# Kernel optimization log

Hardware: AMD Instinct MI355X
Metric: run time of the kernel (lower is better)

## Reference

```python
import jax, jax.numpy as jnp
import numpy as np

DIM = 1024
NUM_HEADS = 16
HEAD_DIM = DIM // NUM_HEADS


def _rope_tables(seq_len, dim, dtype):
    # matches llama_rotary_embedding: inv_freq over even indices of head_dim
    inv_freq = 1.0 / (10000.0 ** (jnp.arange(0, dim, 2, dtype=jnp.float32) / dim))
    t = jnp.arange(seq_len, dtype=jnp.float32)
    freqs = jnp.outer(t, inv_freq)  # [S, dim/2]
    return jnp.cos(freqs).astype(dtype), jnp.sin(freqs).astype(dtype)


def _apply_rope(x, cos_emb, sin_emb):
    # x: [B, H, S, hd]; takes interleaved halves, concatenates rotated halves
    x1 = x[..., 0::2]
    x2 = x[..., 1::2]
    return jnp.concatenate((x1 * cos_emb - x2 * sin_emb,
                            x1 * sin_emb + x2 * cos_emb), axis=-1)


def setup_inputs() -> dict:
    key = jax.random.key(0)
    k_x, k_qkv, k_out, k_b = jax.random.split(key, 4)
    B, S, D = 2, 2048, DIM
    x = jax.random.normal(k_x, (B, S, D), dtype=jnp.float32)
    # torch nn.Linear weights are [out_features, in_features]
    w_qkv = jax.random.normal(k_qkv, (3 * D, D), dtype=jnp.float32) * (1.0 / np.sqrt(D))
    w_out = jax.random.normal(k_out, (D, D), dtype=jnp.float32) * (1.0 / np.sqrt(D))
    b_out = jax.random.normal(k_b, (D,), dtype=jnp.float32) * 0.01
    return {"x": x, "w_qkv": w_qkv, "w_out": w_out, "b_out": b_out}


def reference(x, w_qkv, w_out, b_out):
    B, S, D = x.shape
    H, hd = NUM_HEADS, HEAD_DIM
    qkv = jnp.einsum('bsd,ed->bse', x, w_qkv)  # [B, S, 3D]
    q, k, v = jnp.split(qkv, 3, axis=-1)
    # [B, S, D] -> [B, H, S, hd]
    q, k, v = (t.reshape(B, S, H, hd).transpose(0, 2, 1, 3) for t in (q, k, v))
    cos_emb, sin_emb = _rope_tables(S, hd, x.dtype)  # [S, hd/2]
    q = _apply_rope(q, cos_emb, sin_emb)
    k = _apply_rope(k, cos_emb, sin_emb)
    scores = jnp.einsum('bhqd,bhkd->bhqk', q, k) / jnp.sqrt(jnp.asarray(hd, x.dtype))
    attn = jax.nn.softmax(scores, axis=-1)
    out = jnp.einsum('bhqk,bhkd->bhqd', attn, v)
    out = out.transpose(0, 2, 1, 3).reshape(B, S, D)
    return jnp.einsum('bsd,ed->bse', out, w_out) + b_out
```

## Files before the change

kernel.cpp:

```cpp
#include <hip/hip_runtime.h>
#include <math.h>

typedef __bf16 bf16_t;
typedef bf16_t bf16x8 __attribute__((ext_vector_type(8)));
typedef bf16_t bf16x4 __attribute__((ext_vector_type(4)));
typedef short  s16x4  __attribute__((ext_vector_type(4)));
typedef float  f32x4  __attribute__((ext_vector_type(4)));

#define DIM_   1024
#define NHEADS 16
#define HDIM   64
#define SEQ    2048
#define BATCH  2

#define QK_SCALE 0.18033688011112042f
#define ROPE_LF 0.41524101186092029f

__device__ __forceinline__ s16x4 as_s16x4(bf16x4 v) {
    union { bf16x4 b; s16x4 s; } u; u.b = v; return u.s;
}

__device__ __forceinline__ void gld16(const bf16_t* g, bf16_t* l) {
    __builtin_amdgcn_global_load_lds(
        (const __attribute__((address_space(1))) void*)g,
        (__attribute__((address_space(3))) void*)l, 16, 0, 0);
}

#define XCNT   (4096u * 1024u)
#define WQCNT  (3072u * 1024u)
#define WOCNT  (1024u * 1024u)
__global__ __launch_bounds__(256) void cast3(const float* __restrict__ s0,
                                             const float* __restrict__ s1,
                                             const float* __restrict__ s2,
                                             bf16_t* __restrict__ d0,
                                             bf16_t* __restrict__ d1,
                                             bf16_t* __restrict__ d2) {
    size_t i = ((size_t)blockIdx.x * 256 + threadIdx.x) * 8;
    const float* s; bf16_t* d; size_t off;
    if (i < XCNT)               { s = s0; d = d0; off = i; }
    else if (i < XCNT + WQCNT)  { s = s1; d = d1; off = i - XCNT; }
    else                        { s = s2; d = d2; off = i - XCNT - WQCNT; }
    float4 a = *(const float4*)(s + off);
    float4 b = *(const float4*)(s + off + 4);
    bf16x8 o = { (bf16_t)a.x, (bf16_t)a.y, (bf16_t)a.z, (bf16_t)a.w,
                 (bf16_t)b.x, (bf16_t)b.y, (bf16_t)b.z, (bf16_t)b.w };
    *(bf16x8*)(d + off) = o;
}

__global__ __launch_bounds__(256) void gemm_qkv(const bf16_t* __restrict__ A,
                                                const bf16_t* __restrict__ B,
                                                bf16_t* __restrict__ qb,
                                                bf16_t* __restrict__ kt,
                                                bf16_t* __restrict__ vt,
                                                int M, int N, int K) {
    __shared__ __align__(16) bf16_t As[2][128 * 32];
    __shared__ __align__(16) bf16_t Bs[2][128 * 32];
    const int tid  = threadIdx.x;
    const int m0   = blockIdx.y * 128;
    const int n0   = blockIdx.x * 128;
    const int w    = tid >> 6;
    const int lane = tid & 63;
    const int m16  = lane & 15;
    const int quad = lane >> 4;
    const int wm   = (w >> 1) * 64;
    const int wn   = (w & 1) * 64;
    const int lrow = lane >> 2;
    const int lcol = (lane & 3) * 8;

    const bf16_t* pa0 = A + (size_t)(m0 + w * 16 + lrow) * K + lcol;
    const bf16_t* pb0 = B + (size_t)(n0 + w * 16 + lrow) * K + lcol;
    const int sOffA0 = (w * 16) * 32;
    const int sOffA1 = (64 + w * 16) * 32;

    gld16(pa0, (bf16_t*)As + sOffA0);
    gld16(pa0 + (size_t)64 * K, (bf16_t*)As + sOffA1);
    gld16(pb0, (bf16_t*)Bs + sOffA0);
    gld16(pb0 + (size_t)64 * K, (bf16_t*)Bs + sOffA1);
    __syncthreads();

    f32x4 acc[4][4] = {};
    int buf = 0;

    for (int k0 = 0; k0 < K; k0 += 32) {
        const int nb = buf ^ 1;
        if (k0 + 32 < K) {
            gld16(pa0 + k0 + 32, (bf16_t*)As + nb * 4096 + sOffA0);
            gld16(pa0 + (size_t)64 * K + k0 + 32, (bf16_t*)As + nb * 4096 + sOffA1);
            gld16(pb0 + k0 + 32, (bf16_t*)Bs + nb * 4096 + sOffA0);
            gld16(pb0 + (size_t)64 * K + k0 + 32, (bf16_t*)Bs + nb * 4096 + sOffA1);
        }
        const bf16_t* sA = (const bf16_t*)As + buf * 4096;
        const bf16_t* sB = (const bf16_t*)Bs + buf * 4096;
        bf16x8 af[4], bfr[4];
#pragma unroll
        for (int i = 0; i < 4; ++i)
            af[i] = *(const bf16x8*)(sA + (wm + i * 16 + m16) * 32 + quad * 8);
#pragma unroll
        for (int j = 0; j < 4; ++j)
            bfr[j] = *(const bf16x8*)(sB + (wn + j * 16 + m16) * 32 + quad * 8);
#pragma unroll
        for (int i = 0; i < 4; ++i)
#pragma unroll
            for (int j = 0; j < 4; ++j)
                acc[i][j] = __builtin_amdgcn_mfma_f32_16x16x32_bf16(af[i], bfr[j], acc[i][j], 0, 0, 0);
        __syncthreads();
        buf = nb;
    }

    const int b = m0 >> 11;
    if (n0 < 2 * DIM_) {
        const bool isq = (n0 < DIM_);
        const int  sg  = (m0 & (SEQ - 1)) + wm;
        const float osc = isq ? QK_SCALE : 1.0f;
        const bool even = ((m16 & 1) == 0);
#pragma unroll
        for (int j = 0; j < 4; ++j) {
            const int n = (n0 & (DIM_ - 1)) + wn + j * 16 + m16;
            const int h = n >> 6;
            const int t = (n & 63) >> 1;
            const int dout = even ? t : 32 + t;
            const float freq = exp2f(-ROPE_LF * (float)t);
            float stp_s, stp_c;
            sincosf(freq, &stp_s, &stp_c);
#pragma unroll
            for (int i = 0; i < 4; ++i) {
                float sa, ca;
                sincosf((float)(sg + i * 16 + quad * 4) * freq, &sa, &ca);
#pragma unroll
                for (int r = 0; r < 4; ++r) {
                    const float mine  = acc[i][j][r];
                    const float other = __shfl_xor(mine, 1);
                    const float outv  = (mine * ca + (even ? -other : other) * sa) * osc;
                    if (isq) {
                        qb[(size_t)(m0 + wm + i * 16 + quad * 4 + r) * DIM_ + h * 64 + dout] = (bf16_t)outv;
                    } else {
                        kt[((size_t)(b * 16 + h) * SEQ + (sg + i * 16 + quad * 4 + r)) * 64 + dout] = (bf16_t)outv;
                    }
                    const float nc = ca * stp_c - sa * stp_s;
                    sa = sa * stp_c + ca * stp_s;
                    ca = nc;
                }
            }
        }
    } else {
#pragma unroll
        for (int j = 0; j < 4; ++j) {
            const int n = n0 - 2 * DIM_ + wn + j * 16 + m16;
            const int h = n >> 6;
            const int d = n & 63;
#pragma unroll
            for (int i = 0; i < 4; ++i) {
                const int s0 = (m0 & (SEQ - 1)) + wm + i * 16;
                const int kb = s0 >> 4;
                bf16x4 ov = { (bf16_t)acc[i][j][0], (bf16_t)acc[i][j][1],
                              (bf16_t)acc[i][j][2], (bf16_t)acc[i][j][3] };
                *(bf16x4*)(vt + ((size_t)((b * 16 + h) * 128 + kb) * 64 + d) * 16 + quad * 4) = ov;
            }
        }
    }
}

__global__ __launch_bounds__(256) void gemm_out64(const bf16_t* __restrict__ A,
                                                  const bf16_t* __restrict__ B,
                                                  const float* __restrict__ bias,
                                                  float* __restrict__ C,
                                                  int M, int N, int K) {
    __shared__ __align__(16) bf16_t As[2][128 * 32];
    __shared__ __align__(16) bf16_t Bs[2][64 * 32];
    const int tid  = threadIdx.x;
    const int m0   = blockIdx.y * 128;
    const int n0   = blockIdx.x * 64;
    const int w    = tid >> 6;
    const int lane = tid & 63;
    const int m16  = lane & 15;
    const int quad = lane >> 4;
    const int wm   = (w >> 1) * 64;
    const int wn   = (w & 1) * 32;
    const int lrow = lane >> 2;
    const int lcol = (lane & 3) * 8;

    const bf16_t* pa0 = A + (size_t)(m0 + w * 16 + lrow) * K + lcol;
    const bf16_t* pb0 = B + (size_t)(n0 + w * 16 + lrow) * K + lcol;
    const int sOff0 = (w * 16) * 32;
    const int sOff1 = (64 + w * 16) * 32;

    gld16(pa0, (bf16_t*)As + sOff0);
    gld16(pa0 + (size_t)64 * K, (bf16_t*)As + sOff1);
    gld16(pb0, (bf16_t*)Bs + sOff0);
    __syncthreads();

    f32x4 acc[4][2] = {};
    int buf = 0;

    for (int k0 = 0; k0 < K; k0 += 32) {
        const int nb = buf ^ 1;
        if (k0 + 32 < K) {
            gld16(pa0 + k0 + 32, (bf16_t*)As + nb * 4096 + sOff0);
            gld16(pa0 + (size_t)64 * K + k0 + 32, (bf16_t*)As + nb * 4096 + sOff1);
            gld16(pb0 + k0 + 32, (bf16_t*)Bs + nb * 2048 + sOff0);
        }
        const bf16_t* sA = (const bf16_t*)As + buf * 4096;
        const bf16_t* sB = (const bf16_t*)Bs + buf * 2048;
        bf16x8 af[4], bfr[2];
#pragma unroll
        for (int i = 0; i < 4; ++i)
            af[i] = *(const bf16x8*)(sA + (wm + i * 16 + m16) * 32 + quad * 8);
#pragma unroll
        for (int j = 0; j < 2; ++j)
            bfr[j] = *(const bf16x8*)(sB + (wn + j * 16 + m16) * 32 + quad * 8);
#pragma unroll
        for (int i = 0; i < 4; ++i)
#pragma unroll
            for (int j = 0; j < 2; ++j)
                acc[i][j] = __builtin_amdgcn_mfma_f32_16x16x32_bf16(af[i], bfr[j], acc[i][j], 0, 0, 0);
        __syncthreads();
        buf = nb;
    }

#pragma unroll
    for (int j = 0; j < 2; ++j) {
        const int col = n0 + wn + j * 16 + m16;
        const float bv = bias[col];
#pragma unroll
        for (int i = 0; i < 4; ++i)
#pragma unroll
            for (int r = 0; r < 4; ++r)
                C[(size_t)(m0 + wm + i * 16 + quad * 4 + r) * N + col] = acc[i][j][r] + bv;
    }
}

__global__ __launch_bounds__(256) void attn_mfma(const bf16_t* __restrict__ qb,
                                                 const bf16_t* __restrict__ kt,
                                                 const bf16_t* __restrict__ vt,
                                                 bf16_t* __restrict__ out) {
    __shared__ __align__(16) char smem[17664];
    float* Ored = (float*)smem;
    float* Lred = (float*)(smem + 16640);

    const int tid  = threadIdx.x;
    const int w    = tid >> 6;
    const int lane = tid & 63;
    const int m16  = lane & 15;
    const int quad = lane >> 4;

    const int bid = blockIdx.x;
    const int swz = (bid & 7) * 128 + (bid >> 3);
    const int bh  = swz >> 5;
    const int q0  = (swz & 31) * 64;
    const int b   = bh >> 4;
    const int hh  = bh & 15;

    bf16x8 qf[4][2];
#pragma unroll
    for (int n = 0; n < 4; ++n)
#pragma unroll
        for (int c = 0; c < 2; ++c)
            qf[n][c] = *(const bf16x8*)(qb + (size_t)(b * SEQ + q0 + n * 16 + m16) * DIM_ +
                                        hh * HDIM + c * 32 + quad * 8);

    f32x4 o[4][4] = {};
    float lp[4] = {};

    const bf16_t* kp = kt + ((size_t)bh * SEQ + w * 16 + m16) * 64 + quad * 8;
    const bf16_t* vp = vt + (((size_t)bh * 128 + w) * 64 + m16) * 16 + quad * 4;

#define LOAD_TILE(AK0, AK1, VA)                                \
    do {                                                       \
        AK0 = *(const bf16x8*)(kp);                            \
        AK1 = *(const bf16x8*)(kp + 32);                       \
        VA[0] = *(const bf16x4*)(vp);                          \
        VA[1] = *(const bf16x4*)(vp + 256);                    \
        VA[2] = *(const bf16x4*)(vp + 512);                    \
        VA[3] = *(const bf16x4*)(vp + 768);                    \
        kp += 4096; vp += 4096;                                \
    } while (0)

#define COMPUTE_TILE(AK0, AK1, VA)                                                 \
    do {                                                                           \
        s16x4 pb[4];                                                               \
        _Pragma("unroll")                                                          \
        for (int n = 0; n < 4; ++n) {                                              \
            f32x4 c = {};                                                          \
            c = __builtin_amdgcn_mfma_f32_16x16x32_bf16(AK0, qf[n][0], c, 0, 0, 0); \
            c = __builtin_amdgcn_mfma_f32_16x16x32_bf16(AK1, qf[n][1], c, 0, 0, 0); \
            bf16x4 pv;                                                             \
            _Pragma("unroll")                                                      \
            for (int r = 0; r < 4; ++r) {                                          \
                const float pp = __builtin_amdgcn_exp2f(c[r]);                     \
                lp[n] += pp;                                                       \
                pv[r] = (bf16_t)pp;                                                \
            }                                                                      \
            pb[n] = as_s16x4(pv);                                                  \
        }                                                                          \
        __builtin_amdgcn_s_setprio(1);                                             \
        _Pragma("unroll")                                                          \
        for (int ds = 0; ds < 4; ++ds)                                             \
            _Pragma("unroll")                                                      \
            for (int n = 0; n < 4; ++n)                                            \
                o[ds][n] = __builtin_amdgcn_mfma_f32_16x16x16bf16_1k(               \
                    as_s16x4(VA[ds]), pb[n], o[ds][n], 0, 0, 0);                   \
        __builtin_amdgcn_s_setprio(0);                                             \
    } while (0)

    bf16x8 akA0, akA1, akB0, akB1;
    bf16x4 vaA[4], vaB[4];

    LOAD_TILE(akA0, akA1, vaA);
    for (int t = 0; t < 32; t += 2) {
        LOAD_TILE(akB0, akB1, vaB);
        COMPUTE_TILE(akA0, akA1, vaA);
        if (t + 2 < 32)
            LOAD_TILE(akA0, akA1, vaA);
        COMPUTE_TILE(akB0, akB1, vaB);
    }
#undef LOAD_TILE
#undef COMPUTE_TILE

#pragma unroll
    for (int n = 0; n < 4; ++n) {
        lp[n] += __shfl_xor(lp[n], 16);
        lp[n] += __shfl_xor(lp[n], 32);
    }
    if (quad == 0) {
#pragma unroll
        for (int n = 0; n < 4; ++n) Lred[w * 64 + n * 16 + m16] = lp[n];
    }
    __syncthreads();
    const float linv = 1.0f / (Lred[lane] + Lred[64 + lane] + Lred[128 + lane] + Lred[192 + lane]);

    const size_t obase = (size_t)(b * SEQ + q0 + lane) * DIM_ + hh * HDIM;
#pragma unroll
    for (int p = 0; p < 4; ++p) {
        __syncthreads();
#pragma unroll
        for (int n = 0; n < 4; ++n)
#pragma unroll
            for (int r = 0; r < 4; ++r)
                Ored[w * 1040 + (quad * 4 + r) * 65 + n * 16 + m16] = o[p][n][r];
        __syncthreads();
        union { bf16_t e[4]; bf16x4 v; } ob;
#pragma unroll
        for (int d = 0; d < 4; ++d) {
            const int dd = w * 4 + d;
            const float v = Ored[dd * 65 + lane] + Ored[1040 + dd * 65 + lane] +
                            Ored[2080 + dd * 65 + lane] + Ored[3120 + dd * 65 + lane];
            ob.e[d] = (bf16_t)(v * linv);
        }
        *(bf16x4*)(out + obase + p * 16 + w * 4) = ob.v;
    }
}

extern "C" void kernel_launch(void* const* d_in, const int* in_sizes, int n_in,
                              void* d_out, int out_size, void* d_ws, size_t ws_size,
                              hipStream_t stream) {
    const float* x     = (const float*)d_in[0];
    const float* w_qkv = (const float*)d_in[1];
    const float* w_out = (const float*)d_in[2];
    const float* b_out = (const float*)d_in[3];
    float* out = (float*)d_out;

    const int M = BATCH * SEQ;

    bf16_t* q_b    = (bf16_t*)d_ws;
    bf16_t* attn_b = q_b + (size_t)M * DIM_;
    bf16_t* kt_b   = attn_b + (size_t)M * DIM_;
    bf16_t* vt_b   = kt_b + (size_t)M * DIM_;
    bf16_t* xb     = vt_b + (size_t)M * DIM_;
    bf16_t* wqkvb  = xb + (size_t)M * DIM_;
    bf16_t* woutb  = wqkvb + (size_t)3 * DIM_ * DIM_;

    cast3<<<(XCNT + WQCNT + WOCNT) / (256 * 8), 256, 0, stream>>>(
        x, w_qkv, w_out, xb, wqkvb, woutb);

    gemm_qkv<<<dim3(3 * DIM_ / 128, M / 128), 256, 0, stream>>>(
        xb, wqkvb, q_b, kt_b, vt_b, M, 3 * DIM_, DIM_);

    attn_mfma<<<SEQ / 64 * BATCH * NHEADS, 256, 0, stream>>>(q_b, kt_b, vt_b, attn_b);

    gemm_out64<<<dim3(DIM_ / 64, M / 128), 256, 0, stream>>>(
        attn_b, woutb, b_out, out, M, DIM_, DIM_);
}
```

Before: 198.8 us.

## Enlarge QKV GEMM tiles to 256x256 with triple-buffered swizzled LDS pipeline

The QKV projection GEMM moves from 128x128 tiles with 256 threads to 256x256 tiles with 512 threads, each wave computing a 128x64 sub-tile. The shared-memory pipeline goes from double to triple buffering with explicit vmcnt waits and raw barriers, an XOR swizzle on LDS columns to avoid bank conflicts, and raised priority around the MFMA block. The aim is more operand reuse per load and better overlap of global loads with compute. The cost is 96KB of LDS and a larger accumulator set, which lowers occupancy, and the grid shrinks to 192 blocks, which may underfill the GPU's compute units.

```diff
diff --git a/kernel.cpp b/kernel.cpp
--- a/kernel.cpp
+++ b/kernel.cpp
@@ -47,83 +47,102 @@
     *(bf16x8*)(d + off) = o;
 }
 
-__global__ __launch_bounds__(256) void gemm_qkv(const bf16_t* __restrict__ A,
+__global__ __launch_bounds__(512) void gemm_qkv(const bf16_t* __restrict__ A,
                                                 const bf16_t* __restrict__ B,
                                                 bf16_t* __restrict__ qb,
                                                 bf16_t* __restrict__ kt,
-                                                bf16_t* __restrict__ vt,
-                                                int M, int N, int K) {
-    __shared__ __align__(16) bf16_t As[2][128 * 32];
-    __shared__ __align__(16) bf16_t Bs[2][128 * 32];
+                                                bf16_t* __restrict__ vt) {
+    __shared__ __align__(16) bf16_t smem[3 * 16384];
+
     const int tid  = threadIdx.x;
-    const int m0   = blockIdx.y * 128;
-    const int n0   = blockIdx.x * 128;
-    const int w    = tid >> 6;
+    const int wv   = tid >> 6;
     const int lane = tid & 63;
     const int m16  = lane & 15;
     const int quad = lane >> 4;
-    const int wm   = (w >> 1) * 64;
-    const int wn   = (w & 1) * 64;
-    const int lrow = lane >> 2;
-    const int lcol = (lane & 3) * 8;
-
-    const bf16_t* pa0 = A + (size_t)(m0 + w * 16 + lrow) * K + lcol;
-    const bf16_t* pb0 = B + (size_t)(n0 + w * 16 + lrow) * K + lcol;
-    const int sOffA0 = (w * 16) * 32;
-    const int sOffA1 = (64 + w * 16) * 32;
-
-    gld16(pa0, (bf16_t*)As + sOffA0);
-    gld16(pa0 + (size_t)64 * K, (bf16_t*)As + sOffA1);
-    gld16(pb0, (bf16_t*)Bs + sOffA0);
-    gld16(pb0 + (size_t)64 * K, (bf16_t*)Bs + sOffA1);
-    __syncthreads();
-
-    f32x4 acc[4][4] = {};
-    int buf = 0;
-
-    for (int k0 = 0; k0 < K; k0 += 32) {
-        const int nb = buf ^ 1;
-        if (k0 + 32 < K) {
-            gld16(pa0 + k0 + 32, (bf16_t*)As + nb * 4096 + sOffA0);
-            gld16(pa0 + (size_t)64 * K + k0 + 32, (bf16_t*)As + nb * 4096 + sOffA1);
-            gld16(pb0 + k0 + 32, (bf16_t*)Bs + nb * 4096 + sOffA0);
-            gld16(pb0 + (size_t)64 * K + k0 + 32, (bf16_t*)Bs + nb * 4096 + sOffA1);
-        }
-        const bf16_t* sA = (const bf16_t*)As + buf * 4096;
-        const bf16_t* sB = (const bf16_t*)Bs + buf * 4096;
-        bf16x8 af[4], bfr[4];
-#pragma unroll
-        for (int i = 0; i < 4; ++i)
-            af[i] = *(const bf16x8*)(sA + (wm + i * 16 + m16) * 32 + quad * 8);
+    const int wr   = wv >> 2;
+    const int wc   = wv & 3;
+    const int m0   = blockIdx.y * 256;
+    const int n0   = blockIdx.x * 256;
+    const int K    = 1024;
+    const int NT   = 32;
+
+    const int l2  = lane >> 2;
+    const int scb = (lane & 3) ^ ((lane >> 3) & 3);
+    const int ar0 = wv * 16 + l2;
+    const int ar1 = 128 + ar0;
+    const bf16_t* apA = A + (size_t)(m0 + ar0) * K + scb * 8;
+    const bf16_t* apB = A + (size_t)(m0 + ar1) * K + scb * 8;
+    const bf16_t* bpA = B + (size_t)(n0 + ar0) * K + scb * 8;
+    const bf16_t* bpB = B + (size_t)(n0 + ar1) * K + scb * 8;
+    const int aoffA = (wv * 16) * 32;
+    const int aoffB = (128 + wv * 16) * 32;
+
+#define STAGE(T)                                                   \
+    do {                                                           \
+        bf16_t* sb = smem + ((T) % 3) * 16384;                     \
+        const size_t ko = (size_t)(T) * 32;                        \
+        gld16(apA + ko, sb + aoffA);                               \
+        gld16(apB + ko, sb + aoffB);                               \
+        gld16(bpA + ko, sb + 8192 + aoffA);                        \
+        gld16(bpB + ko, sb + 8192 + aoffB);                        \
+    } while (0)
+
+    f32x4 acc[8][4] = {};
+
+    const int fxor  = (m16 >> 1) & 3;
+    const int abase = (wr * 128 + m16) * 32 + (quad ^ fxor) * 8;
+    const int bbase = (wc * 64 + m16) * 32 + (quad ^ fxor) * 8;
+
+    STAGE(0);
+    STAGE(1);
+    asm volatile("s_waitcnt vmcnt(4)" ::: "memory");
+    __builtin_amdgcn_s_barrier();
+    __builtin_amdgcn_sched_barrier(0);
+
+    for (int t = 0; t < NT; ++t) {
+        if (t + 2 < NT) STAGE(t + 2);
+        const bf16_t* sA = smem + (t % 3) * 16384;
+        const bf16_t* sB = sA + 8192;
+        bf16x8 af[8], bfr[4];
+#pragma unroll
+        for (int i = 0; i < 8; ++i)
+            af[i] = *(const bf16x8*)(sA + abase + i * 512);
 #pragma unroll
         for (int j = 0; j < 4; ++j)
-            bfr[j] = *(const bf16x8*)(sB + (wn + j * 16 + m16) * 32 + quad * 8);
-#pragma unroll
-        for (int i = 0; i < 4; ++i)
+            bfr[j] = *(const bf16x8*)(sB + bbase + j * 512);
+        __builtin_amdgcn_s_setprio(1);
+#pragma unroll
+        for (int i = 0; i < 8; ++i)
 #pragma unroll
             for (int j = 0; j < 4; ++j)
                 acc[i][j] = __builtin_amdgcn_mfma_f32_16x16x32_bf16(af[i], bfr[j], acc[i][j], 0, 0, 0);
-        __syncthreads();
-        buf = nb;
-    }
+        __builtin_amdgcn_s_setprio(0);
+        if (t < NT - 1) {
+            if (t < NT - 2) asm volatile("s_waitcnt vmcnt(4)" ::: "memory");
+            else            asm volatile("s_waitcnt vmcnt(0)" ::: "memory");
+            __builtin_amdgcn_s_barrier();
+            __builtin_amdgcn_sched_barrier(0);
+        }
+    }
+#undef STAGE
 
     const int b = m0 >> 11;
     if (n0 < 2 * DIM_) {
         const bool isq = (n0 < DIM_);
-        const int  sg  = (m0 & (SEQ - 1)) + wm;
+        const int  sg  = (m0 & (SEQ - 1)) + wr * 128;
         const float osc = isq ? QK_SCALE : 1.0f;
         const bool even = ((m16 & 1) == 0);
 #pragma unroll
         for (int j = 0; j < 4; ++j) {
-            const int n = (n0 & (DIM_ - 1)) + wn + j * 16 + m16;
+            const int n = (n0 & (DIM_ - 1)) + wc * 64 + j * 16 + m16;
             const int h = n >> 6;
-            const int t = (n & 63) >> 1;
-            const int dout = even ? t : 32 + t;
-            const float freq = exp2f(-ROPE_LF * (float)t);
+            const int tt = (n & 63) >> 1;
+            const int dout = even ? tt : 32 + tt;
+            const float freq = exp2f(-ROPE_LF * (float)tt);
             float stp_s, stp_c;
             sincosf(freq, &stp_s, &stp_c);
 #pragma unroll
-            for (int i = 0; i < 4; ++i) {
+            for (int i = 0; i < 8; ++i) {
                 float sa, ca;
                 sincosf((float)(sg + i * 16 + quad * 4) * freq, &sa, &ca);
 #pragma unroll
@@ -132,7 +151,7 @@
                     const float other = __shfl_xor(mine, 1);
                     const float outv  = (mine * ca + (even ? -other : other) * sa) * osc;
                     if (isq) {
-                        qb[(size_t)(m0 + wm + i * 16 + quad * 4 + r) * DIM_ + h * 64 + dout] = (bf16_t)outv;
+                        qb[(size_t)(m0 + wr * 128 + i * 16 + quad * 4 + r) * DIM_ + h * 64 + dout] = (bf16_t)outv;
                     } else {
                         kt[((size_t)(b * 16 + h) * SEQ + (sg + i * 16 + quad * 4 + r)) * 64 + dout] = (bf16_t)outv;
                     }
@@ -145,12 +164,12 @@
     } else {
 #pragma unroll
         for (int j = 0; j < 4; ++j) {
-            const int n = n0 - 2 * DIM_ + wn + j * 16 + m16;
+            const int n = n0 - 2 * DIM_ + wc * 64 + j * 16 + m16;
             const int h = n >> 6;
             const int d = n & 63;
 #pragma unroll
-            for (int i = 0; i < 4; ++i) {
-                const int s0 = (m0 & (SEQ - 1)) + wm + i * 16;
+            for (int i = 0; i < 8; ++i) {
+                const int s0 = (m0 & (SEQ - 1)) + wr * 128 + i * 16;
                 const int kb = s0 >> 4;
                 bf16x4 ov = { (bf16_t)acc[i][j][0], (bf16_t)acc[i][j][1],
                               (bf16_t)acc[i][j][2], (bf16_t)acc[i][j][3] };
@@ -372,8 +391,8 @@
     cast3<<<(XCNT + WQCNT + WOCNT) / (256 * 8), 256, 0, stream>>>(
         x, w_qkv, w_out, xb, wqkvb, woutb);
 
-    gemm_qkv<<<dim3(3 * DIM_ / 128, M / 128), 256, 0, stream>>>(
-        xb, wqkvb, q_b, kt_b, vt_b, M, 3 * DIM_, DIM_);
+    gemm_qkv<<<dim3(3 * DIM_ / 256, M / 256), 512, 0, stream>>>(
+        xb, wqkvb, q_b, kt_b, vt_b);
 
     attn_mfma<<<SEQ / 64 * BATCH * NHEADS, 256, 0, stream>>>(q_b, kt_b, vt_b, attn_b);
 
```

After: 205.9 us. +3.6%, slower.
